# Kernel tuning notes

Measured on AMD Instinct MI355X. Metric: run time of the kernel, lower is better.

The kernel has to match this reference:

```python
import jax, jax.numpy as jnp
import numpy as np

N, S, D_IN, ATTN_DIM, OUT_DIM = 4, 8192, 1024, 1024, 1024


def setup_inputs() -> dict:
    key = jax.random.key(0)
    ks = jax.random.split(key, 6)
    scale_in = 1.0 / np.sqrt(D_IN)
    scale_attn = 1.0 / np.sqrt(ATTN_DIM)
    return {
        "x": jax.random.normal(ks[0], (N, S, D_IN), dtype=jnp.float32),
        "wq": jax.random.normal(ks[1], (D_IN, ATTN_DIM), dtype=jnp.float32) * scale_in,
        "bq": jnp.zeros((ATTN_DIM,), dtype=jnp.float32),
        "wk": jax.random.normal(ks[2], (D_IN, ATTN_DIM), dtype=jnp.float32) * scale_in,
        "bk": jnp.zeros((ATTN_DIM,), dtype=jnp.float32),
        "wv": jax.random.normal(ks[3], (D_IN, ATTN_DIM), dtype=jnp.float32) * scale_in,
        "bv": jnp.zeros((ATTN_DIM,), dtype=jnp.float32),
        "wo": jax.random.normal(ks[4], (ATTN_DIM, OUT_DIM), dtype=jnp.float32) * scale_attn,
        "bo": jnp.zeros((OUT_DIM,), dtype=jnp.float32),
    }


def reference(x, wq, bq, wk, bk, wv, bv, wo, bo):
    # QKV projections (Dense layers)
    query = x @ wq + bq  # [n, s, h]
    key_ = x @ wk + bk
    value = x @ wv + bv
    # elu+1 feature map
    Q = jax.nn.elu(query) + 1.0
    K = jax.nn.elu(key_) + 1.0
    # per-channel global reductions over sequence (einsum 'nsh,nsh->nh')
    KV = jnp.einsum('nsh,nsh->nh', K, value, precision='highest')  # [n, h]
    Ksum = jnp.sum(K, axis=1)  # [n, h]
    Z = 1.0 / (Q * Ksum[:, None, :] + 1e-6)  # [n, s, h]
    V = Q * KV[:, None, :] * Z  # [n, s, h]
    out = V @ wo + bo
    return jax.nn.gelu(out, approximate=True)
```

## Files before the change

kernel.cpp:

```cpp
#include <hip/hip_runtime.h>
#include <math.h>
#include <stdint.h>


#define S_LEN 8192
#define M_TOT 32768

typedef __attribute__((ext_vector_type(8))) __bf16 bf16x8;
typedef __attribute__((ext_vector_type(8))) unsigned short ushort8;
typedef __attribute__((ext_vector_type(4))) float f32x4;

__device__ __forceinline__ unsigned short f2bf(float f) {
    unsigned int u = __builtin_bit_cast(unsigned int, f);
    unsigned int r = (u + 0x7fffu + ((u >> 16) & 1u)) >> 16;
    return (unsigned short)r;
}
__device__ __forceinline__ float bf2f(unsigned short s) {
    unsigned int u = ((unsigned int)s) << 16;
    return __builtin_bit_cast(float, u);
}
__device__ __forceinline__ float elu1(float v) { return v > 0.f ? v + 1.f : __expf(v); }
__device__ __forceinline__ float gelu_tanh(float v) {
    float u = 1.5957691216057308f * (v + 0.044715f * v * v * v);
    float e = __expf(u);
    float th = 1.f - 2.f / (e + 1.f);
    return 0.5f * v * (1.f + th);
}

__device__ __forceinline__ void glds16(const void* g, void* l) {
    __builtin_amdgcn_global_load_lds(
        (const __attribute__((address_space(1))) unsigned int*)(uintptr_t)g,
        (__attribute__((address_space(3))) unsigned int*)(uintptr_t)l, 16, 0, 0);
}

__global__ __launch_bounds__(256) void xconv(const float* __restrict__ x,
                                             unsigned short* __restrict__ xb)
{
    const size_t base = ((size_t)blockIdx.x * 256 + threadIdx.x) * 8;
    float4 a = *(const float4*)&x[base];
    float4 b = *(const float4*)&x[base + 4];
    ushort8 o;
    o[0] = f2bf(a.x); o[1] = f2bf(a.y); o[2] = f2bf(a.z); o[3] = f2bf(a.w);
    o[4] = f2bf(b.x); o[5] = f2bf(b.y); o[6] = f2bf(b.z); o[7] = f2bf(b.w);
    *(ushort8*)&xb[base] = o;
}

__global__ __launch_bounds__(256) void wtrans(const float* __restrict__ w,
                                              unsigned short* __restrict__ wT)
{
    __shared__ float tile[64][65];
    const int t  = threadIdx.x;
    const int n0 = blockIdx.x * 64;
    const int k0 = blockIdx.y * 64;
    const int r  = t >> 2;
    const int c4 = (t & 3) * 16;
    #pragma unroll
    for (int j = 0; j < 4; ++j) {
        float4 v = *(const float4*)&w[(size_t)(k0 + r) * 1024 + n0 + c4 + j * 4];
        tile[r][c4 + j * 4 + 0] = v.x; tile[r][c4 + j * 4 + 1] = v.y;
        tile[r][c4 + j * 4 + 2] = v.z; tile[r][c4 + j * 4 + 3] = v.w;
    }
    __syncthreads();
    const int nn = t >> 2;
    const int kc = (t & 3) * 16;
    ushort8 o0, o1;
    #pragma unroll
    for (int j = 0; j < 8; ++j) o0[j] = f2bf(tile[kc + j][nn]);
    #pragma unroll
    for (int j = 0; j < 8; ++j) o1[j] = f2bf(tile[kc + 8 + j][nn]);
    *(ushort8*)&wT[(size_t)(n0 + nn) * 1024 + k0 + kc]     = o0;
    *(ushort8*)&wT[(size_t)(n0 + nn) * 1024 + k0 + kc + 8] = o1;
}

__global__ __launch_bounds__(256) void qkv_mfma(
    const unsigned short* __restrict__ xb,
    const unsigned short* __restrict__ wqT,
    const unsigned short* __restrict__ wkT,
    const unsigned short* __restrict__ wvT,
    const float* __restrict__ bq, const float* __restrict__ bk,
    const float* __restrict__ bv,
    unsigned short* __restrict__ Qout,
    float* __restrict__ KV, float* __restrict__ Ks,
    int moff)
{
    __shared__ unsigned short Alds[128 * 64];
    __shared__ unsigned short Blds[3][64 * 64];
    __shared__ float redkv[8][64];
    __shared__ float redks[8][64];

    const int t  = threadIdx.x;
    const int h0 = blockIdx.x * 64;
    const int m0 = blockIdx.y * 128;
    const int mg = moff + m0;
    const int n  = mg >> 13;

    const int lane = t & 63, wid = t >> 6;
    const int wm = wid >> 1, wn = wid & 1;
    const int lr = lane & 15, quad = lane >> 4;

    f32x4 accq[4][2], acck[4][2], accv[4][2];
    #pragma unroll
    for (int mi = 0; mi < 4; ++mi)
        #pragma unroll
        for (int nj = 0; nj < 2; ++nj) {
            accq[mi][nj] = (f32x4){0.f, 0.f, 0.f, 0.f};
            acck[mi][nj] = (f32x4){0.f, 0.f, 0.f, 0.f};
            accv[mi][nj] = (f32x4){0.f, 0.f, 0.f, 0.f};
        }

    for (int k0 = 0; k0 < 1024; k0 += 64) {
        __syncthreads();
        #pragma unroll
        for (int i = 0; i < 4; ++i) {
            const int s = wid * 256 + i * 64 + lane;
            const int r = s >> 3;
            const int j = (s & 7) ^ (r & 7);
            glds16(&xb[(size_t)(m0 + r) * 1024 + k0 + j * 8],
                   &Alds[(wid * 256 + i * 64) * 8]);
        }
        #pragma unroll
        for (int i = 0; i < 2; ++i) {
            const int s = wid * 128 + i * 64 + lane;
            const int r = s >> 3;
            const int j = (s & 7) ^ (r & 7);
            const size_t go = (size_t)(h0 + r) * 1024 + k0 + j * 8;
            const int lo = (wid * 128 + i * 64) * 8;
            glds16(&wqT[go], &Blds[0][lo]);
            glds16(&wkT[go], &Blds[1][lo]);
            glds16(&wvT[go], &Blds[2][lo]);
        }
        __syncthreads();
        #pragma unroll
        for (int ks = 0; ks < 2; ++ks) {
            bf16x8 af[4];
            #pragma unroll
            for (int mi = 0; mi < 4; ++mi) {
                const int r = wm * 64 + mi * 16 + lr;
                const int off = r * 64 + (((ks * 4 + quad) ^ (r & 7)) * 8);
                af[mi] = __builtin_bit_cast(bf16x8, *(const ushort8*)&Alds[off]);
            }
            bf16x8 bfq[2], bfk[2], bfv[2];
            #pragma unroll
            for (int nj = 0; nj < 2; ++nj) {
                const int r = wn * 32 + nj * 16 + lr;
                const int off = r * 64 + (((ks * 4 + quad) ^ (r & 7)) * 8);
                bfq[nj] = __builtin_bit_cast(bf16x8, *(const ushort8*)&Blds[0][off]);
                bfk[nj] = __builtin_bit_cast(bf16x8, *(const ushort8*)&Blds[1][off]);
                bfv[nj] = __builtin_bit_cast(bf16x8, *(const ushort8*)&Blds[2][off]);
            }
            #pragma unroll
            for (int mi = 0; mi < 4; ++mi)
                #pragma unroll
                for (int nj = 0; nj < 2; ++nj) {
                    accq[mi][nj] = __builtin_amdgcn_mfma_f32_16x16x32_bf16(af[mi], bfq[nj], accq[mi][nj], 0, 0, 0);
                    acck[mi][nj] = __builtin_amdgcn_mfma_f32_16x16x32_bf16(af[mi], bfk[nj], acck[mi][nj], 0, 0, 0);
                    accv[mi][nj] = __builtin_amdgcn_mfma_f32_16x16x32_bf16(af[mi], bfv[nj], accv[mi][nj], 0, 0, 0);
                }
        }
    }

    float bqv[2], bkv[2], bvv[2];
    #pragma unroll
    for (int nj = 0; nj < 2; ++nj) {
        const int h = h0 + wn * 32 + nj * 16 + lr;
        bqv[nj] = bq[h]; bkv[nj] = bk[h]; bvv[nj] = bv[h];
    }
    float kvp[2] = {0.f, 0.f}, ksp[2] = {0.f, 0.f};
    #pragma unroll
    for (int mi = 0; mi < 4; ++mi)
        #pragma unroll
        for (int nj = 0; nj < 2; ++nj) {
            const int h = h0 + wn * 32 + nj * 16 + lr;
            #pragma unroll
            for (int r = 0; r < 4; ++r) {
                const int m = mg + wm * 64 + mi * 16 + quad * 4 + r;
                float q = elu1(accq[mi][nj][r] + bqv[nj]);
                Qout[(size_t)m * 1024 + h] = f2bf(q);
                float kk = elu1(acck[mi][nj][r] + bkv[nj]);
                float vv = accv[mi][nj][r] + bvv[nj];
                kvp[nj] = fmaf(kk, vv, kvp[nj]);
                ksp[nj] += kk;
            }
        }
    #pragma unroll
    for (int nj = 0; nj < 2; ++nj) {
        redkv[wm * 4 + quad][wn * 32 + nj * 16 + lr] = kvp[nj];
        redks[wm * 4 + quad][wn * 32 + nj * 16 + lr] = ksp[nj];
    }
    __syncthreads();
    if (t < 64) {
        float s = 0.f;
        #pragma unroll
        for (int g = 0; g < 8; ++g) s += redkv[g][t];
        atomicAdd(&KV[n * 1024 + h0 + t], s);
    } else if (t < 128) {
        const int c = t - 64;
        float s = 0.f;
        #pragma unroll
        for (int g = 0; g < 8; ++g) s += redks[g][c];
        atomicAdd(&Ks[n * 1024 + h0 + c], s);
    }
}

__global__ __launch_bounds__(256) void vprime(
    unsigned short* __restrict__ Q,
    const float* __restrict__ KV, const float* __restrict__ Ks)
{
    const size_t idx  = (size_t)blockIdx.x * 256 + threadIdx.x;
    const size_t base = idx * 8;
    const int h = (int)(base & 1023);
    const int n = (int)(base >> 23);
    ushort8 q8 = *(ushort8*)&Q[base];
    const float* kvp = &KV[n * 1024 + h];
    const float* ksp = &Ks[n * 1024 + h];
    ushort8 o;
    #pragma unroll
    for (int j = 0; j < 8; ++j) {
        float qf = bf2f(q8[j]);
        float vp = qf * kvp[j] * __builtin_amdgcn_rcpf(fmaf(qf, ksp[j], 1e-6f));
        o[j] = f2bf(vp);
    }
    *(ushort8*)&Q[base] = o;
}

__global__ __launch_bounds__(256) void out_mfma(
    const unsigned short* __restrict__ Vp,
    const unsigned short* __restrict__ woT,
    const float* __restrict__ bo, float* __restrict__ out)
{
    __shared__ unsigned short Alds[128 * 64];
    __shared__ unsigned short Blds[64 * 64];

    const int t  = threadIdx.x;
    const int h0 = blockIdx.x * 64;
    const int m0 = blockIdx.y * 128;

    const int lane = t & 63, wid = t >> 6;
    const int wm = wid >> 1, wn = wid & 1;
    const int lr = lane & 15, quad = lane >> 4;

    f32x4 acc[4][2];
    #pragma unroll
    for (int mi = 0; mi < 4; ++mi)
        #pragma unroll
        for (int nj = 0; nj < 2; ++nj) acc[mi][nj] = (f32x4){0.f, 0.f, 0.f, 0.f};

    for (int k0 = 0; k0 < 1024; k0 += 64) {
        __syncthreads();
        #pragma unroll
        for (int i = 0; i < 4; ++i) {
            const int s = wid * 256 + i * 64 + lane;
            const int r = s >> 3;
            const int j = (s & 7) ^ (r & 7);
            glds16(&Vp[(size_t)(m0 + r) * 1024 + k0 + j * 8],
                   &Alds[(wid * 256 + i * 64) * 8]);
        }
        #pragma unroll
        for (int i = 0; i < 2; ++i) {
            const int s = wid * 128 + i * 64 + lane;
            const int r = s >> 3;
            const int j = (s & 7) ^ (r & 7);
            glds16(&woT[(size_t)(h0 + r) * 1024 + k0 + j * 8],
                   &Blds[(wid * 128 + i * 64) * 8]);
        }
        __syncthreads();
        #pragma unroll
        for (int ks = 0; ks < 2; ++ks) {
            bf16x8 af[4];
            #pragma unroll
            for (int mi = 0; mi < 4; ++mi) {
                const int r = wm * 64 + mi * 16 + lr;
                const int off = r * 64 + (((ks * 4 + quad) ^ (r & 7)) * 8);
                af[mi] = __builtin_bit_cast(bf16x8, *(const ushort8*)&Alds[off]);
            }
            bf16x8 bf_[2];
            #pragma unroll
            for (int nj = 0; nj < 2; ++nj) {
                const int r = wn * 32 + nj * 16 + lr;
                const int off = r * 64 + (((ks * 4 + quad) ^ (r & 7)) * 8);
                bf_[nj] = __builtin_bit_cast(bf16x8, *(const ushort8*)&Blds[off]);
            }
            #pragma unroll
            for (int mi = 0; mi < 4; ++mi)
                #pragma unroll
                for (int nj = 0; nj < 2; ++nj)
                    acc[mi][nj] = __builtin_amdgcn_mfma_f32_16x16x32_bf16(af[mi], bf_[nj], acc[mi][nj], 0, 0, 0);
        }
    }

    float bov[2];
    #pragma unroll
    for (int nj = 0; nj < 2; ++nj) bov[nj] = bo[h0 + wn * 32 + nj * 16 + lr];
    #pragma unroll
    for (int mi = 0; mi < 4; ++mi)
        #pragma unroll
        for (int nj = 0; nj < 2; ++nj) {
            const int h = h0 + wn * 32 + nj * 16 + lr;
            #pragma unroll
            for (int r = 0; r < 4; ++r) {
                const int m = m0 + wm * 64 + mi * 16 + quad * 4 + r;
                out[(size_t)m * 1024 + h] = gelu_tanh(acc[mi][nj][r] + bov[nj]);
            }
        }
}

extern "C" void kernel_launch(void* const* d_in, const int* in_sizes, int n_in,
                              void* d_out, int out_size, void* d_ws, size_t ws_size,
                              hipStream_t stream)
{
    const float* x  = (const float*)d_in[0];
    const float* wq = (const float*)d_in[1];
    const float* bq = (const float*)d_in[2];
    const float* wk = (const float*)d_in[3];
    const float* bk = (const float*)d_in[4];
    const float* wv = (const float*)d_in[5];
    const float* bv = (const float*)d_in[6];
    const float* wo = (const float*)d_in[7];
    const float* bo = (const float*)d_in[8];
    float* out = (float*)d_out;

    char* wsb = (char*)d_ws;
    unsigned short* Qws = (unsigned short*)wsb;
    unsigned short* xb  = (unsigned short*)(wsb + 67108864ULL);
    unsigned short* wqT = (unsigned short*)(wsb + 100663296ULL);
    unsigned short* wkT = wqT + 1048576;
    unsigned short* wvT = wkT + 1048576;
    unsigned short* woT = wvT + 1048576;
    float* KV = (float*)(wsb + 100663296ULL + 4ULL * 2097152);
    float* Ks = KV + 4 * 1024;

    hipMemsetAsync(KV, 0, 2 * 4 * 1024 * sizeof(float), stream);

    dim3 tg(16, 16);
    wtrans<<<tg, 256, 0, stream>>>(wq, wqT);
    wtrans<<<tg, 256, 0, stream>>>(wk, wkT);
    wtrans<<<tg, 256, 0, stream>>>(wv, wvT);
    wtrans<<<tg, 256, 0, stream>>>(wo, woT);

    for (int half = 0; half < 2; ++half) {
        xconv<<<8192, 256, 0, stream>>>(x + (size_t)half * 16384 * 1024, xb);
        qkv_mfma<<<dim3(16, 128), 256, 0, stream>>>(xb, wqT, wkT, wvT, bq, bk, bv,
                                                    Qws, KV, Ks, half * 16384);
    }
    vprime<<<16384, 256, 0, stream>>>(Qws, KV, Ks);
    out_mfma<<<dim3(16, 256), 256, 0, stream>>>(Qws, woT, bo, out);
}
```

Measured before the change: 576.0 us.

## Double-buffer and interleave LDS loads with MFMA in both GEMM kernels

Rewrites the QKV and output GEMMs as 512-thread blocks with double-buffered LDS. Global-to-LDS staging for the next k-tile is issued between MFMA phases, using explicit waitcnt, barriers and setprio to overlap loads with compute. The output GEMM tile grows to 256x256 with 8x4 accumulators per wave to increase reuse. The four weight-transpose launches are merged into one. The gains come at the cost of more LDS and registers per block, which lowers occupancy, and of fragile hand-placed synchronization.

```diff
diff --git a/kernel.cpp b/kernel.cpp
--- a/kernel.cpp
+++ b/kernel.cpp
@@ -4,7 +4,6 @@
 
 
 #define S_LEN 8192
-#define M_TOT 32768
 
 typedef __attribute__((ext_vector_type(8))) __bf16 bf16x8;
 typedef __attribute__((ext_vector_type(8))) unsigned short ushort8;
@@ -26,12 +25,17 @@
     float th = 1.f - 2.f / (e + 1.f);
     return 0.5f * v * (1.f + th);
 }
-
 __device__ __forceinline__ void glds16(const void* g, void* l) {
     __builtin_amdgcn_global_load_lds(
         (const __attribute__((address_space(1))) unsigned int*)(uintptr_t)g,
         (__attribute__((address_space(3))) unsigned int*)(uintptr_t)l, 16, 0, 0);
 }
+
+#define KBAR()  asm volatile("s_barrier" ::: "memory")
+#define LGKM0() do { asm volatile("s_waitcnt lgkmcnt(0)" ::: "memory"); \
+                     __builtin_amdgcn_sched_barrier(0); } while (0)
+#define VM2()   asm volatile("s_waitcnt vmcnt(2)" ::: "memory")
+#define VM0()   asm volatile("s_waitcnt vmcnt(0)" ::: "memory")
 
 __global__ __launch_bounds__(256) void xconv(const float* __restrict__ x,
                                              unsigned short* __restrict__ xb)
@@ -45,10 +49,16 @@
     *(ushort8*)&xb[base] = o;
 }
 
-__global__ __launch_bounds__(256) void wtrans(const float* __restrict__ w,
+__global__ __launch_bounds__(256) void wtrans(const float* __restrict__ wq,
+                                              const float* __restrict__ wk,
+                                              const float* __restrict__ wv,
+                                              const float* __restrict__ wo,
                                               unsigned short* __restrict__ wT)
 {
     __shared__ float tile[64][65];
+    const int z = blockIdx.z;
+    const float* w = (z == 0) ? wq : (z == 1) ? wk : (z == 2) ? wv : wo;
+    unsigned short* dst = wT + (size_t)z * 1048576;
     const int t  = threadIdx.x;
     const int n0 = blockIdx.x * 64;
     const int k0 = blockIdx.y * 64;
@@ -68,11 +78,11 @@
     for (int j = 0; j < 8; ++j) o0[j] = f2bf(tile[kc + j][nn]);
     #pragma unroll
     for (int j = 0; j < 8; ++j) o1[j] = f2bf(tile[kc + 8 + j][nn]);
-    *(ushort8*)&wT[(size_t)(n0 + nn) * 1024 + k0 + kc]     = o0;
-    *(ushort8*)&wT[(size_t)(n0 + nn) * 1024 + k0 + kc + 8] = o1;
-}
-
-__global__ __launch_bounds__(256) void qkv_mfma(
+    *(ushort8*)&dst[(size_t)(n0 + nn) * 1024 + k0 + kc]     = o0;
+    *(ushort8*)&dst[(size_t)(n0 + nn) * 1024 + k0 + kc + 8] = o1;
+}
+
+__global__ __launch_bounds__(512) void qkv_mfma(
     const unsigned short* __restrict__ xb,
     const unsigned short* __restrict__ wqT,
     const unsigned short* __restrict__ wkT,
@@ -83,20 +93,40 @@
     float* __restrict__ KV, float* __restrict__ Ks,
     int moff)
 {
-    __shared__ unsigned short Alds[128 * 64];
-    __shared__ unsigned short Blds[3][64 * 64];
-    __shared__ float redkv[8][64];
-    __shared__ float redks[8][64];
-
-    const int t  = threadIdx.x;
-    const int h0 = blockIdx.x * 64;
-    const int m0 = blockIdx.y * 128;
-    const int mg = moff + m0;
-    const int n  = mg >> 13;
+    __shared__ unsigned short Alds[2][256 * 64];
+    __shared__ unsigned short Blds[3][2][64 * 64];
+    __shared__ float redkv[16][64];
+    __shared__ float redks[16][64];
+
+    const int t    = threadIdx.x;
+    const int h0   = blockIdx.x * 64;
+    const int m0   = blockIdx.y * 256;
+    const int mg   = moff + m0;
+    const int bidx = mg >> 13;
 
     const int lane = t & 63, wid = t >> 6;
     const int wm = wid >> 1, wn = wid & 1;
     const int lr = lane & 15, quad = lane >> 4;
+
+    const int sA   = wid * 64 + lane;
+    const int xks0 = ((quad)     ^ (lr & 7)) * 8;
+    const int xks1 = ((quad | 4) ^ (lr & 7)) * 8;
+    const int arow = (wm * 64 + lr) * 64;
+    const int brow = (wn * 32 + lr) * 64;
+
+    auto stA = [&](int kt, int u, int buf) {
+        const int s = u * 512 + sA;
+        const int r = s >> 3;
+        const int j = (s & 7) ^ (r & 7);
+        glds16(&xb[(size_t)(m0 + r) * 1024 + kt * 64 + j * 8],
+               &Alds[buf][(u * 512 + wid * 64) * 8]);
+    };
+    auto stB = [&](const unsigned short* w, int mat, int kt, int buf) {
+        const int r = sA >> 3;
+        const int j = (sA & 7) ^ (r & 7);
+        glds16(&w[(size_t)(h0 + r) * 1024 + kt * 64 + j * 8],
+               &Blds[mat][buf][(wid * 64) * 8]);
+    };
 
     f32x4 accq[4][2], acck[4][2], accv[4][2];
     #pragma unroll
@@ -108,56 +138,75 @@
             accv[mi][nj] = (f32x4){0.f, 0.f, 0.f, 0.f};
         }
 
-    for (int k0 = 0; k0 < 1024; k0 += 64) {
-        __syncthreads();
-        #pragma unroll
-        for (int i = 0; i < 4; ++i) {
-            const int s = wid * 256 + i * 64 + lane;
-            const int r = s >> 3;
-            const int j = (s & 7) ^ (r & 7);
-            glds16(&xb[(size_t)(m0 + r) * 1024 + k0 + j * 8],
-                   &Alds[(wid * 256 + i * 64) * 8]);
-        }
-        #pragma unroll
-        for (int i = 0; i < 2; ++i) {
-            const int s = wid * 128 + i * 64 + lane;
-            const int r = s >> 3;
-            const int j = (s & 7) ^ (r & 7);
-            const size_t go = (size_t)(h0 + r) * 1024 + k0 + j * 8;
-            const int lo = (wid * 128 + i * 64) * 8;
-            glds16(&wqT[go], &Blds[0][lo]);
-            glds16(&wkT[go], &Blds[1][lo]);
-            glds16(&wvT[go], &Blds[2][lo]);
-        }
-        __syncthreads();
-        #pragma unroll
-        for (int ks = 0; ks < 2; ++ks) {
-            bf16x8 af[4];
-            #pragma unroll
-            for (int mi = 0; mi < 4; ++mi) {
-                const int r = wm * 64 + mi * 16 + lr;
-                const int off = r * 64 + (((ks * 4 + quad) ^ (r & 7)) * 8);
-                af[mi] = __builtin_bit_cast(bf16x8, *(const ushort8*)&Alds[off]);
-            }
-            bf16x8 bfq[2], bfk[2], bfv[2];
-            #pragma unroll
-            for (int nj = 0; nj < 2; ++nj) {
-                const int r = wn * 32 + nj * 16 + lr;
-                const int off = r * 64 + (((ks * 4 + quad) ^ (r & 7)) * 8);
-                bfq[nj] = __builtin_bit_cast(bf16x8, *(const ushort8*)&Blds[0][off]);
-                bfk[nj] = __builtin_bit_cast(bf16x8, *(const ushort8*)&Blds[1][off]);
-                bfv[nj] = __builtin_bit_cast(bf16x8, *(const ushort8*)&Blds[2][off]);
-            }
-            #pragma unroll
-            for (int mi = 0; mi < 4; ++mi)
-                #pragma unroll
-                for (int nj = 0; nj < 2; ++nj) {
-                    accq[mi][nj] = __builtin_amdgcn_mfma_f32_16x16x32_bf16(af[mi], bfq[nj], accq[mi][nj], 0, 0, 0);
-                    acck[mi][nj] = __builtin_amdgcn_mfma_f32_16x16x32_bf16(af[mi], bfk[nj], acck[mi][nj], 0, 0, 0);
-                    accv[mi][nj] = __builtin_amdgcn_mfma_f32_16x16x32_bf16(af[mi], bfv[nj], accv[mi][nj], 0, 0, 0);
-                }
-        }
-    }
+    #pragma unroll
+    for (int u = 0; u < 4; ++u) stA(0, u, 0);
+    stB(wqT, 0, 0, 0); stB(wkT, 1, 0, 0); stB(wvT, 2, 0, 0);
+    stA(1, 0, 1); stA(1, 1, 1);
+    VM2();
+    KBAR();
+
+    bf16x8 af[4];
+
+#define QKV_LDA(BUF, XK)                                                        \
+    {                                                                           \
+        _Pragma("unroll")                                                       \
+        for (int mi = 0; mi < 4; ++mi)                                          \
+            af[mi] = __builtin_bit_cast(bf16x8,                                 \
+                *(const ushort8*)&Alds[BUF][arow + mi * 1024 + (XK)]);          \
+    }
+
+#define QKV_PHASE(BUF, NJ, XK, STG, WT)                                         \
+    {                                                                           \
+        bf16x8 b0 = __builtin_bit_cast(bf16x8,                                  \
+            *(const ushort8*)&Blds[0][BUF][brow + (NJ) * 1024 + (XK)]);         \
+        bf16x8 b1 = __builtin_bit_cast(bf16x8,                                  \
+            *(const ushort8*)&Blds[1][BUF][brow + (NJ) * 1024 + (XK)]);         \
+        bf16x8 b2 = __builtin_bit_cast(bf16x8,                                  \
+            *(const ushort8*)&Blds[2][BUF][brow + (NJ) * 1024 + (XK)]);         \
+        STG;                                                                    \
+        KBAR();                                                                 \
+        LGKM0();                                                                \
+        __builtin_amdgcn_s_setprio(1);                                          \
+        _Pragma("unroll")                                                       \
+        for (int mi = 0; mi < 4; ++mi) {                                        \
+            accq[mi][NJ] = __builtin_amdgcn_mfma_f32_16x16x32_bf16(af[mi], b0, accq[mi][NJ], 0, 0, 0); \
+            acck[mi][NJ] = __builtin_amdgcn_mfma_f32_16x16x32_bf16(af[mi], b1, acck[mi][NJ], 0, 0, 0); \
+            accv[mi][NJ] = __builtin_amdgcn_mfma_f32_16x16x32_bf16(af[mi], b2, accv[mi][NJ], 0, 0, 0); \
+        }                                                                       \
+        __builtin_amdgcn_s_setprio(0);                                          \
+        WT;                                                                     \
+        KBAR();                                                                 \
+    }
+
+    for (int i = 0; i < 8; ++i) {
+        const int t1 = 2 * i + 1;
+        QKV_LDA(0, xks0);
+        QKV_PHASE(0, 0, xks0, { stA(t1, 2, 1); stA(t1, 3, 1); }, {});
+        QKV_PHASE(0, 1, xks0, { stB(wqT, 0, t1, 1); stB(wkT, 1, t1, 1); }, {});
+        QKV_LDA(0, xks1);
+        QKV_PHASE(0, 0, xks1, { stB(wvT, 2, t1, 1); }, {});
+        if (i < 7) {
+            QKV_PHASE(0, 1, xks1, { stA(t1 + 1, 0, 0); stA(t1 + 1, 1, 0); }, VM2());
+        } else {
+            QKV_PHASE(0, 1, xks1, {}, VM0());
+        }
+        QKV_LDA(1, xks0);
+        if (i < 7) {
+            QKV_PHASE(1, 0, xks0, { stA(t1 + 1, 2, 0); stA(t1 + 1, 3, 0); }, {});
+            QKV_PHASE(1, 1, xks0, { stB(wqT, 0, t1 + 1, 0); stB(wkT, 1, t1 + 1, 0); }, {});
+            QKV_LDA(1, xks1);
+            QKV_PHASE(1, 0, xks1, { stB(wvT, 2, t1 + 1, 0); }, {});
+            QKV_PHASE(1, 1, xks1, { stA(t1 + 2, 0, 1); stA(t1 + 2, 1, 1); }, VM2());
+        } else {
+            QKV_PHASE(1, 0, xks0, {}, {});
+            QKV_PHASE(1, 1, xks0, {}, {});
+            QKV_LDA(1, xks1);
+            QKV_PHASE(1, 0, xks1, {}, {});
+            QKV_PHASE(1, 1, xks1, {}, {});
+        }
+    }
+#undef QKV_LDA
+#undef QKV_PHASE
 
     float bqv[2], bkv[2], bvv[2];
     #pragma unroll
@@ -191,14 +240,14 @@
     if (t < 64) {
         float s = 0.f;
         #pragma unroll
-        for (int g = 0; g < 8; ++g) s += redkv[g][t];
-        atomicAdd(&KV[n * 1024 + h0 + t], s);
+        for (int g = 0; g < 16; ++g) s += redkv[g][t];
+        atomicAdd(&KV[bidx * 1024 + h0 + t], s);
     } else if (t < 128) {
         const int c = t - 64;
         float s = 0.f;
         #pragma unroll
-        for (int g = 0; g < 8; ++g) s += redks[g][c];
-        atomicAdd(&Ks[n * 1024 + h0 + c], s);
+        for (int g = 0; g < 16; ++g) s += redks[g][c];
+        atomicAdd(&Ks[bidx * 1024 + h0 + c], s);
     }
 }
 
@@ -223,83 +272,150 @@
     *(ushort8*)&Q[base] = o;
 }
 
-__global__ __launch_bounds__(256) void out_mfma(
+__global__ __launch_bounds__(512) void out_mfma(
     const unsigned short* __restrict__ Vp,
     const unsigned short* __restrict__ woT,
     const float* __restrict__ bo, float* __restrict__ out)
 {
-    __shared__ unsigned short Alds[128 * 64];
-    __shared__ unsigned short Blds[64 * 64];
+    __shared__ unsigned short Alds[2][256 * 64];
+    __shared__ unsigned short Blds[2][256 * 64];
 
     const int t  = threadIdx.x;
-    const int h0 = blockIdx.x * 64;
-    const int m0 = blockIdx.y * 128;
+    const int h0 = blockIdx.x * 256;
+    const int m0 = blockIdx.y * 256;
 
     const int lane = t & 63, wid = t >> 6;
-    const int wm = wid >> 1, wn = wid & 1;
+    const int wm = wid >> 2, wn = wid & 3;
     const int lr = lane & 15, quad = lane >> 4;
 
-    f32x4 acc[4][2];
-    #pragma unroll
-    for (int mi = 0; mi < 4; ++mi)
-        #pragma unroll
-        for (int nj = 0; nj < 2; ++nj) acc[mi][nj] = (f32x4){0.f, 0.f, 0.f, 0.f};
-
-    for (int k0 = 0; k0 < 1024; k0 += 64) {
-        __syncthreads();
-        #pragma unroll
-        for (int i = 0; i < 4; ++i) {
-            const int s = wid * 256 + i * 64 + lane;
-            const int r = s >> 3;
-            const int j = (s & 7) ^ (r & 7);
-            glds16(&Vp[(size_t)(m0 + r) * 1024 + k0 + j * 8],
-                   &Alds[(wid * 256 + i * 64) * 8]);
-        }
-        #pragma unroll
-        for (int i = 0; i < 2; ++i) {
-            const int s = wid * 128 + i * 64 + lane;
-            const int r = s >> 3;
-            const int j = (s & 7) ^ (r & 7);
-            glds16(&woT[(size_t)(h0 + r) * 1024 + k0 + j * 8],
-                   &Blds[(wid * 128 + i * 64) * 8]);
-        }
-        __syncthreads();
-        #pragma unroll
-        for (int ks = 0; ks < 2; ++ks) {
-            bf16x8 af[4];
-            #pragma unroll
-            for (int mi = 0; mi < 4; ++mi) {
-                const int r = wm * 64 + mi * 16 + lr;
-                const int off = r * 64 + (((ks * 4 + quad) ^ (r & 7)) * 8);
-                af[mi] = __builtin_bit_cast(bf16x8, *(const ushort8*)&Alds[off]);
-            }
-            bf16x8 bf_[2];
-            #pragma unroll
-            for (int nj = 0; nj < 2; ++nj) {
-                const int r = wn * 32 + nj * 16 + lr;
-                const int off = r * 64 + (((ks * 4 + quad) ^ (r & 7)) * 8);
-                bf_[nj] = __builtin_bit_cast(bf16x8, *(const ushort8*)&Blds[off]);
-            }
-            #pragma unroll
-            for (int mi = 0; mi < 4; ++mi)
-                #pragma unroll
-                for (int nj = 0; nj < 2; ++nj)
-                    acc[mi][nj] = __builtin_amdgcn_mfma_f32_16x16x32_bf16(af[mi], bf_[nj], acc[mi][nj], 0, 0, 0);
-        }
-    }
-
-    float bov[2];
-    #pragma unroll
-    for (int nj = 0; nj < 2; ++nj) bov[nj] = bo[h0 + wn * 32 + nj * 16 + lr];
-    #pragma unroll
-    for (int mi = 0; mi < 4; ++mi)
-        #pragma unroll
-        for (int nj = 0; nj < 2; ++nj) {
-            const int h = h0 + wn * 32 + nj * 16 + lr;
+    const int sA   = wid * 64 + lane;
+    const int xks0 = ((quad)     ^ (lr & 7)) * 8;
+    const int xks1 = ((quad | 4) ^ (lr & 7)) * 8;
+    const int arow = (wm * 128 + lr) * 64;
+    const int brow = (wn * 64 + lr) * 64;
+
+    auto stA = [&](int kt, int u, int buf) {
+        const int s = u * 512 + sA;
+        const int r = s >> 3;
+        const int j = (s & 7) ^ (r & 7);
+        glds16(&Vp[(size_t)(m0 + r) * 1024 + kt * 64 + j * 8],
+               &Alds[buf][(u * 512 + wid * 64) * 8]);
+    };
+    auto stB = [&](int kt, int u, int buf) {
+        const int s = u * 512 + sA;
+        const int r = s >> 3;
+        const int j = (s & 7) ^ (r & 7);
+        glds16(&woT[(size_t)(h0 + r) * 1024 + kt * 64 + j * 8],
+               &Blds[buf][(u * 512 + wid * 64) * 8]);
+    };
+
+    f32x4 acc[8][4];
+    #pragma unroll
+    for (int mr = 0; mr < 8; ++mr)
+        #pragma unroll
+        for (int nc = 0; nc < 4; ++nc) acc[mr][nc] = (f32x4){0.f, 0.f, 0.f, 0.f};
+
+    #pragma unroll
+    for (int u = 0; u < 4; ++u) stA(0, u, 0);
+    #pragma unroll
+    for (int u = 0; u < 4; ++u) stB(0, u, 0);
+    stA(1, 0, 1); stA(1, 1, 1);
+    VM2();
+    KBAR();
+
+    bf16x8 af[4][2], bf_[2][2];
+
+#define OUT_LDA(BUF, MH)                                                        \
+    {                                                                           \
+        _Pragma("unroll")                                                       \
+        for (int mi = 0; mi < 4; ++mi) {                                        \
+            af[mi][0] = __builtin_bit_cast(bf16x8,                              \
+                *(const ushort8*)&Alds[BUF][arow + (MH) * 4096 + mi * 1024 + xks0]); \
+            af[mi][1] = __builtin_bit_cast(bf16x8,                              \
+                *(const ushort8*)&Alds[BUF][arow + (MH) * 4096 + mi * 1024 + xks1]); \
+        }                                                                       \
+    }
+
+#define OUT_LDB(BUF, NH)                                                        \
+    {                                                                           \
+        _Pragma("unroll")                                                       \
+        for (int nj = 0; nj < 2; ++nj) {                                        \
+            bf_[nj][0] = __builtin_bit_cast(bf16x8,                             \
+                *(const ushort8*)&Blds[BUF][brow + (NH) * 2048 + nj * 1024 + xks0]); \
+            bf_[nj][1] = __builtin_bit_cast(bf16x8,                             \
+                *(const ushort8*)&Blds[BUF][brow + (NH) * 2048 + nj * 1024 + xks1]); \
+        }                                                                       \
+    }
+
+#define OUT_PHASE(MH, NH, STG, WT)                                              \
+    {                                                                           \
+        STG;                                                                    \
+        KBAR();                                                                 \
+        LGKM0();                                                                \
+        __builtin_amdgcn_s_setprio(1);                                          \
+        _Pragma("unroll")                                                       \
+        for (int mi = 0; mi < 4; ++mi)                                          \
+            _Pragma("unroll")                                                   \
+            for (int nj = 0; nj < 2; ++nj) {                                    \
+                acc[(MH) * 4 + mi][(NH) * 2 + nj] = __builtin_amdgcn_mfma_f32_16x16x32_bf16( \
+                    af[mi][0], bf_[nj][0], acc[(MH) * 4 + mi][(NH) * 2 + nj], 0, 0, 0); \
+                acc[(MH) * 4 + mi][(NH) * 2 + nj] = __builtin_amdgcn_mfma_f32_16x16x32_bf16( \
+                    af[mi][1], bf_[nj][1], acc[(MH) * 4 + mi][(NH) * 2 + nj], 0, 0, 0); \
+            }                                                                   \
+        __builtin_amdgcn_s_setprio(0);                                          \
+        WT;                                                                     \
+        KBAR();                                                                 \
+    }
+
+    for (int i = 0; i < 8; ++i) {
+        const int t1 = 2 * i + 1;
+        OUT_LDA(0, 0); OUT_LDB(0, 0);
+        OUT_PHASE(0, 0, { stA(t1, 2, 1); stA(t1, 3, 1); }, {});
+        OUT_LDB(0, 1);
+        OUT_PHASE(0, 1, { stB(t1, 0, 1); stB(t1, 1, 1); }, {});
+        OUT_LDA(0, 1);
+        OUT_PHASE(1, 1, { stB(t1, 2, 1); stB(t1, 3, 1); }, {});
+        OUT_LDB(0, 0);
+        if (i < 7) {
+            OUT_PHASE(1, 0, { stA(t1 + 1, 0, 0); stA(t1 + 1, 1, 0); }, VM2());
+        } else {
+            OUT_PHASE(1, 0, {}, VM0());
+        }
+        OUT_LDA(1, 0); OUT_LDB(1, 0);
+        if (i < 7) {
+            OUT_PHASE(0, 0, { stA(t1 + 1, 2, 0); stA(t1 + 1, 3, 0); }, {});
+            OUT_LDB(1, 1);
+            OUT_PHASE(0, 1, { stB(t1 + 1, 0, 0); stB(t1 + 1, 1, 0); }, {});
+            OUT_LDA(1, 1);
+            OUT_PHASE(1, 1, { stB(t1 + 1, 2, 0); stB(t1 + 1, 3, 0); }, {});
+            OUT_LDB(1, 0);
+            OUT_PHASE(1, 0, { stA(t1 + 2, 0, 1); stA(t1 + 2, 1, 1); }, VM2());
+        } else {
+            OUT_PHASE(0, 0, {}, {});
+            OUT_LDB(1, 1);
+            OUT_PHASE(0, 1, {}, {});
+            OUT_LDA(1, 1);
+            OUT_PHASE(1, 1, {}, {});
+            OUT_LDB(1, 0);
+            OUT_PHASE(1, 0, {}, {});
+        }
+    }
+#undef OUT_LDA
+#undef OUT_LDB
+#undef OUT_PHASE
+
+    float bov[4];
+    #pragma unroll
+    for (int nc = 0; nc < 4; ++nc) bov[nc] = bo[h0 + wn * 64 + nc * 16 + lr];
+    #pragma unroll
+    for (int mr = 0; mr < 8; ++mr)
+        #pragma unroll
+        for (int nc = 0; nc < 4; ++nc) {
+            const int h = h0 + wn * 64 + nc * 16 + lr;
             #pragma unroll
             for (int r = 0; r < 4; ++r) {
-                const int m = m0 + wm * 64 + mi * 16 + quad * 4 + r;
-                out[(size_t)m * 1024 + h] = gelu_tanh(acc[mi][nj][r] + bov[nj]);
+                const int m = m0 + wm * 128 + mr * 16 + quad * 4 + r;
+                out[(size_t)m * 1024 + h] = gelu_tanh(acc[mr][nc][r] + bov[nc]);
             }
         }
 }
@@ -331,17 +447,13 @@
 
     hipMemsetAsync(KV, 0, 2 * 4 * 1024 * sizeof(float), stream);
 
-    dim3 tg(16, 16);
-    wtrans<<<tg, 256, 0, stream>>>(wq, wqT);
-    wtrans<<<tg, 256, 0, stream>>>(wk, wkT);
-    wtrans<<<tg, 256, 0, stream>>>(wv, wvT);
-    wtrans<<<tg, 256, 0, stream>>>(wo, woT);
+    wtrans<<<dim3(16, 16, 4), 256, 0, stream>>>(wq, wk, wv, wo, wqT);
 
     for (int half = 0; half < 2; ++half) {
         xconv<<<8192, 256, 0, stream>>>(x + (size_t)half * 16384 * 1024, xb);
-        qkv_mfma<<<dim3(16, 128), 256, 0, stream>>>(xb, wqT, wkT, wvT, bq, bk, bv,
-                                                    Qws, KV, Ks, half * 16384);
+        qkv_mfma<<<dim3(16, 64), 512, 0, stream>>>(xb, wqT, wkT, wvT, bq, bk, bv,
+                                                   Qws, KV, Ks, half * 16384);
     }
     vprime<<<16384, 256, 0, stream>>>(Qws, KV, Ks);
-    out_mfma<<<dim3(16, 256), 256, 0, stream>>>(Qws, woT, bo, out);
-}
+    out_mfma<<<dim3(4, 128), 512, 0, stream>>>(Qws, woT, bo, out);
+}
```

Measured after the change: 532.3 us. -7.6%, faster.
